# Optimization experiments

Hardware: AMD Instinct MI355X
Metric: run time of the kernel (lower is better)

## Reference

```python
import jax, jax.numpy as jnp
import numpy as np

T, D, H, HD = 2048, 2048, 16, 128
ROPE_BASE = 10000.0
NEG = jnp.float32(-1e30)


def rms_norm(x):
    # F.rms_norm(x, (x.size(-1),)) with default eps = dtype eps
    eps = jnp.finfo(x.dtype).eps
    return x * jax.lax.rsqrt(jnp.mean(x * x, axis=-1, keepdims=True) + eps)


def rotary(x):
    # x: [1, T, H, hd]; half-split rotation as in Rotary.forward
    hd = x.shape[-1]
    inv_freq = (1.0 / ROPE_BASE) ** (jnp.arange(0, hd, 2, dtype=jnp.float32) / hd)
    t = jnp.arange(x.shape[1], dtype=jnp.float32)
    freqs = jnp.outer(t, inv_freq)                      # [T, hd/2]
    cos = jnp.cos(freqs)[None, :, None, :]
    sin = jnp.sin(freqs)[None, :, None, :]
    x1, x2 = jnp.split(x, 2, axis=-1)
    return jnp.concatenate([x1 * cos + x2 * sin, -x1 * sin + x2 * cos], axis=-1)


def setup_inputs() -> dict:
    key = jax.random.key(0)
    ks = jax.random.split(key, 10)
    w = lambda k, shape: jax.random.normal(k, shape, jnp.float32) * 0.02
    return {
        "x":  jax.random.normal(ks[0], (1, T, D), jnp.float32),
        "vi": jax.random.normal(ks[1], (1, T, H, HD), jnp.float32),
        "x0": jax.random.normal(ks[2], (1, T, D), jnp.float32),
        "wq": w(ks[3], (D, D)),
        "wk": w(ks[4], (D, D)),
        "wv": w(ks[5], (D, D)),
        "wo": w(ks[6], (D, D)),
        "lamb": jnp.float32(0.5),
        "lambdas": jnp.array([1.0, 0.0], jnp.float32),
        "w_fc": w(ks[7], (4 * D, D)),
        "w_proj": w(ks[8], (D, 4 * D)),
    }


def reference(x, vi, x0, wq, wk, wv, wo, lamb, lambdas, w_fc, w_proj):
    # Block: residual blend with initial embedding x0
    xb = lambdas[0] * x + lambdas[1] * x0
    xn = rms_norm(xb)

    # --- CausalSelfAttention ---
    q = (xn @ wq.T).reshape(1, T, H, HD)
    k = (xn @ wk.T).reshape(1, T, H, HD)
    v = (xn @ wv.T).reshape(1, T, H, HD)
    v = (1.0 - lamb) * v + lamb * vi                     # value-embedding blend
    q = rotary(rms_norm(q))
    k = rotary(rms_norm(k))

    scale = 1.0 / jnp.sqrt(jnp.float32(HD))              # flex_attention default scale
    scores = jnp.einsum('bqhd,bkhd->bhqk', q, k) * scale # [1,H,T,T]
    causal = jnp.tril(jnp.ones((T, T), bool))
    scores = jnp.where(causal[None, None], scores, NEG)
    attn = jax.nn.softmax(scores, axis=-1)
    y = jnp.einsum('bhqk,bkhd->bqhd', attn, v).reshape(1, T, D)
    a = y @ wo.T                                         # attention output REPLACES x (no residual)

    # --- MLP with squared ReLU ---
    h = rms_norm(a) @ w_fc.T
    h = jnp.square(jax.nn.relu(h))
    out = a + h @ w_proj.T
    return out
```

## Files before the change

### kernel.cpp

```cpp
#include <hip/hip_runtime.h>
#include <hip/hip_bf16.h>

typedef __bf16 bf16;
typedef __bf16 bf16x8 __attribute__((ext_vector_type(8)));
typedef float f32x4 __attribute__((ext_vector_type(4)));
typedef unsigned int u32x4 __attribute__((ext_vector_type(4)));

#define DD 2048
#define DD2 4194304ull
#define G9_LDS 131072
#define G10_LDS 65536

__device__ __forceinline__ void glds16(const void* g, void* l) {
  __builtin_amdgcn_global_load_lds((const __attribute__((address_space(1))) void*)g,
                                   (__attribute__((address_space(3))) void*)l, 16, 0, 0);
}

__device__ __forceinline__ f32x4 mfma16(bf16x8 a, bf16x8 b, f32x4 c) {
  return __builtin_amdgcn_mfma_f32_16x16x32_bf16(a, b, c, 0, 0, 0);
}

__device__ __forceinline__ unsigned pk2(float lo, float hi) {
  unsigned short a = __builtin_bit_cast(unsigned short, (bf16)lo);
  unsigned short b = __builtin_bit_cast(unsigned short, (bf16)hi);
  return (unsigned)a | ((unsigned)b << 16);
}

__device__ __forceinline__ void cvt_body(const float* s0, const float* s1, const float* s2,
                                         const float* s3, bf16* dst, int seglog, size_t total,
                                         int bid, int nb) {
  size_t i = ((size_t)bid * 256 + threadIdx.x) * 16;
  const size_t stride = (size_t)nb * 256 * 16;
  for (; i < total; i += stride) {
    int seg = (int)(i >> seglog);
    const float* src = (seg == 0) ? s0 : (seg == 1) ? s1 : (seg == 2) ? s2 : s3;
    size_t loc = i - ((size_t)seg << seglog);
    float4 a0 = *(const float4*)(src + loc);
    float4 a1 = *(const float4*)(src + loc + 4);
    float4 a2 = *(const float4*)(src + loc + 8);
    float4 a3 = *(const float4*)(src + loc + 12);
    bf16x8 o0, o1;
    o0[0] = (bf16)a0.x; o0[1] = (bf16)a0.y; o0[2] = (bf16)a0.z; o0[3] = (bf16)a0.w;
    o0[4] = (bf16)a1.x; o0[5] = (bf16)a1.y; o0[6] = (bf16)a1.z; o0[7] = (bf16)a1.w;
    o1[0] = (bf16)a2.x; o1[1] = (bf16)a2.y; o1[2] = (bf16)a2.z; o1[3] = (bf16)a2.w;
    o1[4] = (bf16)a3.x; o1[5] = (bf16)a3.y; o1[6] = (bf16)a3.z; o1[7] = (bf16)a3.w;
    *(bf16x8*)(dst + i) = o0;
    *(bf16x8*)(dst + i + 8) = o1;
  }
}

__global__ __launch_bounds__(256) void pre_k(const float* __restrict__ wq, const float* __restrict__ wk,
                                             const float* __restrict__ wv, const float* __restrict__ wo,
                                             bf16* __restrict__ wdst,
                                             const float* __restrict__ x, const float* __restrict__ x0,
                                             const float* __restrict__ lambdas, bf16* __restrict__ xn) {
  if (blockIdx.x < 2048) {
    cvt_body(wq, wk, wv, wo, wdst, 22, 4 * DD2, blockIdx.x, 2048);
    return;
  }
  const int t = blockIdx.x - 2048, tid = threadIdx.x;
  const float4* xr = (const float4*)(x + (size_t)t * DD);
  float4 a0 = xr[2 * tid], a1 = xr[2 * tid + 1];
  float v[8] = {a0.x, a0.y, a0.z, a0.w, a1.x, a1.y, a1.z, a1.w};
  const float l0 = lambdas[0], l1 = lambdas[1];
  const float4* yr = (const float4*)(x0 + (size_t)t * DD);
  float4 b0 = yr[2 * tid], b1 = yr[2 * tid + 1];
  float w[8] = {b0.x, b0.y, b0.z, b0.w, b1.x, b1.y, b1.z, b1.w};
#pragma unroll
  for (int i = 0; i < 8; ++i) v[i] = l0 * v[i] + l1 * w[i];
  float ss = 0.f;
#pragma unroll
  for (int i = 0; i < 8; ++i) ss += v[i] * v[i];
#pragma unroll
  for (int off = 1; off < 64; off <<= 1) ss += __shfl_xor(ss, off, 64);
  __shared__ float red[4];
  if ((tid & 63) == 0) red[tid >> 6] = ss;
  __syncthreads();
  ss = red[0] + red[1] + red[2] + red[3];
  const float sc = rsqrtf(ss * (1.0f / DD) + 1.1920928955078125e-07f);
  bf16x8 o;
#pragma unroll
  for (int i = 0; i < 8; ++i) o[i] = (bf16)(v[i] * sc);
  *(bf16x8*)(xn + (size_t)t * DD + tid * 8) = o;
}

__global__ __launch_bounds__(256) void ropevt_k(bf16* __restrict__ qg, bf16* __restrict__ kg,
                                                const bf16* __restrict__ v, bf16* __restrict__ vt) {
  __shared__ alignas(16) bf16 tile[16 * 128];
  if (blockIdx.x < 16384) {
    const int tid = threadIdx.x, lane = tid & 63, wid = tid >> 6;
    const int p = blockIdx.x * 4 + wid;
    bf16* base = ((p >> 15) ? kg : qg);
    const int t = (p >> 4) & 2047, hh = p & 15;
    base += (size_t)t * DD + hh * 128;
    float x1 = (float)base[lane], x2 = (float)base[lane + 64];
    float ss = x1 * x1 + x2 * x2;
#pragma unroll
    for (int off = 1; off < 64; off <<= 1) ss += __shfl_xor(ss, off, 64);
    const float sc = rsqrtf(ss * (1.0f / 128.0f) + 1.1920928955078125e-07f);
    x1 *= sc; x2 *= sc;
    const float fr = (float)t * exp2f((float)lane * (-13.287712379549449f / 64.0f));
    const float s = sinf(fr), c = cosf(fr);
    base[lane]      = (bf16)(x1 * c + x2 * s);
    base[lane + 64] = (bf16)(-x1 * s + x2 * c);
    return;
  }
  const int b = blockIdx.x - 16384;
  const int tb = b & 127, hb = b >> 7, tid = threadIdx.x;
  glds16(v + (size_t)(tb * 16 + (tid >> 4)) * DD + hb * 128 + (tid & 15) * 8, tile + tid * 8);
  __syncthreads();
  const int d_l = tid & 127, tc = tid >> 7;
  bf16x8 o;
#pragma unroll
  for (int i = 0; i < 8; ++i) o[i] = tile[(tc * 8 + i) * 128 + d_l];
  *(bf16x8*)(vt + (size_t)(hb * 128 + d_l) * DD + tb * 16 + tc * 8) = o;
}

__device__ __forceinline__ void g9_stageA(const bf16* A, int Kstride, int row0, int k0,
                                          bf16* buf, int hm, int tid) {
#pragma unroll
  for (int i = 0; i < 2; ++i) {
    int e = tid + i * 512;
    int prl = e >> 3, slot = e & 7;
    int wm = prl >> 6, r63 = prl & 63;
    glds16(A + (size_t)(row0 + wm * 128 + hm * 64 + r63) * Kstride + k0 + ((slot ^ (prl & 7)) * 8),
           buf + hm * 8192 + e * 8);
  }
}
__device__ __forceinline__ void g9_stageB(const bf16* B, int Kstride, int col0, int k0,
                                          bf16* buf, int hn, int tid) {
#pragma unroll
  for (int i = 0; i < 2; ++i) {
    int e = tid + i * 512;
    int pbl = e >> 3, slot = e & 7;
    int wn = pbl >> 5, q = pbl & 31;
    glds16(B + (size_t)(col0 + wn * 64 + hn * 32 + q) * Kstride + k0 + ((slot ^ (pbl & 7)) * 8),
           buf + 16384 + hn * 8192 + e * 8);
  }
}

__device__ __forceinline__ void gemm9_core(const bf16* __restrict__ A, const bf16* __restrict__ B,
                                           int Kstride, int Klen, int row0, int col0,
                                           bf16* smem, f32x4 (&acc)[8][4]) {
  const int tid = threadIdx.x, lane = tid & 63, wid = tid >> 6;
  const int wm = wid >> 2, wn = wid & 3;
  const int l15 = lane & 15, g = lane >> 4;
  const int sw = l15 & 7;
  const int NT = Klen >> 6;
  g9_stageA(A, Kstride, row0, 0, smem, 0, tid);
  g9_stageB(B, Kstride, col0, 0, smem, 0, tid);
  g9_stageB(B, Kstride, col0, 0, smem, 1, tid);
  g9_stageA(A, Kstride, row0, 0, smem, 1, tid);
  g9_stageA(A, Kstride, row0, 64, smem + 32768, 0, tid);
  g9_stageB(B, Kstride, col0, 64, smem + 32768, 0, tid);
  asm volatile("s_waitcnt vmcnt(8)" ::: "memory");
  __builtin_amdgcn_s_barrier();

  bf16x8 a[4][2], b0[2][2], b1[2][2];
  for (int t = 0; t < NT; ++t) {
    bf16* cb = smem + (t & 1) * 32768;
    bf16* nb = smem + ((t + 1) & 1) * 32768;
    const bool s1 = (t + 1) < NT, s2 = (t + 2) < NT;
#pragma unroll
    for (int mm = 0; mm < 4; ++mm)
#pragma unroll
      for (int ks = 0; ks < 2; ++ks)
        a[mm][ks] = *(const bf16x8*)(cb + (wm * 64 + mm * 16 + l15) * 64 + (((ks * 4 + g) ^ sw) * 8));
#pragma unroll
    for (int nn = 0; nn < 2; ++nn)
#pragma unroll
      for (int ks = 0; ks < 2; ++ks)
        b0[nn][ks] = *(const bf16x8*)(cb + 16384 + (wn * 32 + nn * 16 + l15) * 64 + (((ks * 4 + g) ^ sw) * 8));
    if (s1) { g9_stageB(B, Kstride, col0, (t + 1) << 6, nb, 1, tid);
              g9_stageA(A, Kstride, row0, (t + 1) << 6, nb, 1, tid);
              asm volatile("s_waitcnt vmcnt(8)" ::: "memory"); }
    else    { asm volatile("s_waitcnt vmcnt(0)" ::: "memory"); }
    __builtin_amdgcn_s_barrier();
    __builtin_amdgcn_s_setprio(1);
#pragma unroll
    for (int mm = 0; mm < 4; ++mm)
#pragma unroll
      for (int nn = 0; nn < 2; ++nn)
#pragma unroll
        for (int ks = 0; ks < 2; ++ks)
          acc[mm][nn] = mfma16(a[mm][ks], b0[nn][ks], acc[mm][nn]);
    __builtin_amdgcn_s_setprio(0);
#pragma unroll
    for (int nn = 0; nn < 2; ++nn)
#pragma unroll
      for (int ks = 0; ks < 2; ++ks)
        b1[nn][ks] = *(const bf16x8*)(cb + 16384 + 8192 + (wn * 32 + nn * 16 + l15) * 64 + (((ks * 4 + g) ^ sw) * 8));
    __builtin_amdgcn_s_barrier();
    __builtin_amdgcn_s_setprio(1);
#pragma unroll
    for (int mm = 0; mm < 4; ++mm)
#pragma unroll
      for (int nn = 0; nn < 2; ++nn)
#pragma unroll
        for (int ks = 0; ks < 2; ++ks)
          acc[mm][2 + nn] = mfma16(a[mm][ks], b1[nn][ks], acc[mm][2 + nn]);
    __builtin_amdgcn_s_setprio(0);
#pragma unroll
    for (int mm = 0; mm < 4; ++mm)
#pragma unroll
      for (int ks = 0; ks < 2; ++ks)
        a[mm][ks] = *(const bf16x8*)(cb + 8192 + (wm * 64 + mm * 16 + l15) * 64 + (((ks * 4 + g) ^ sw) * 8));
    __builtin_amdgcn_s_barrier();
    __builtin_amdgcn_s_setprio(1);
#pragma unroll
    for (int mm = 0; mm < 4; ++mm)
#pragma unroll
      for (int nn = 0; nn < 2; ++nn)
#pragma unroll
        for (int ks = 0; ks < 2; ++ks)
          acc[4 + mm][nn] = mfma16(a[mm][ks], b0[nn][ks], acc[4 + mm][nn]);
    __builtin_amdgcn_s_setprio(0);
    if (s2) { g9_stageA(A, Kstride, row0, (t + 2) << 6, cb, 0, tid);
              g9_stageB(B, Kstride, col0, (t + 2) << 6, cb, 0, tid);
              asm volatile("s_waitcnt vmcnt(8)" ::: "memory"); }
    else if (s1) { asm volatile("s_waitcnt vmcnt(4)" ::: "memory"); }
    __builtin_amdgcn_s_barrier();
    __builtin_amdgcn_s_setprio(1);
#pragma unroll
    for (int mm = 0; mm < 4; ++mm)
#pragma unroll
      for (int nn = 0; nn < 2; ++nn)
#pragma unroll
        for (int ks = 0; ks < 2; ++ks)
          acc[4 + mm][2 + nn] = mfma16(a[mm][ks], b1[nn][ks], acc[4 + mm][2 + nn]);
    __builtin_amdgcn_s_setprio(0);
  }
}

#define GEMM9_EPI(STMT)                                                        \
  { const int lane_ = threadIdx.x & 63, wid_ = threadIdx.x >> 6;               \
    const int l15_ = lane_ & 15, g_ = lane_ >> 4;                              \
    const int wm_ = wid_ >> 2, wn_ = wid_ & 3;                                 \
    _Pragma("unroll") for (int m = 0; m < 8; ++m)                              \
    _Pragma("unroll") for (int n = 0; n < 4; ++n)                              \
    _Pragma("unroll") for (int j = 0; j < 4; ++j) {                            \
      int grow = row0 + wm_ * 128 + (m >> 2) * 64 + (m & 3) * 16 + g_ * 4 + j; \
      int gcol = col0 + wn_ * 64 + (n >> 1) * 32 + (n & 1) * 16 + l15_;        \
      float vacc = acc[m][n][j];                                               \
      STMT; } }

__global__ __launch_bounds__(512, 1) void gemm9_qkv(const bf16* __restrict__ A,
    const bf16* __restrict__ Wq, const bf16* __restrict__ Wk, const bf16* __restrict__ Wv,
    bf16* __restrict__ oq, bf16* __restrict__ ok, bf16* __restrict__ ov,
    const float* __restrict__ vi, const float* __restrict__ lambp) {
  extern __shared__ bf16 smem9[];
  const int z = blockIdx.z;
  const bf16* B = (z == 0) ? Wq : (z == 1) ? Wk : Wv;
  bf16* out = (z == 0) ? oq : (z == 1) ? ok : ov;
  const int row0 = blockIdx.y * 256, col0 = blockIdx.x * 256;
  f32x4 acc[8][4] = {};
  gemm9_core(A, B, DD, DD, row0, col0, smem9, acc);
  if (z < 2) {
    GEMM9_EPI( out[(size_t)grow * DD + gcol] = (bf16)vacc; )
  } else {
    const float lam = *lambp;
    GEMM9_EPI( out[(size_t)grow * DD + gcol] =
                 (bf16)((1.0f - lam) * vacc + lam * vi[(size_t)grow * DD + gcol]); )
  }
}

__global__ __launch_bounds__(512, 1) void gemm9_relu(const bf16* __restrict__ A, const bf16* __restrict__ B,
                                                     bf16* __restrict__ out, int N, int Kstride, int Klen) {
  extern __shared__ bf16 smem9[];
  const int row0 = blockIdx.y * 256, col0 = blockIdx.x * 256;
  f32x4 acc[8][4] = {};
  gemm9_core(A, B, Kstride, Klen, row0, col0, smem9, acc);
  GEMM9_EPI( float r = fmaxf(vacc, 0.f); out[(size_t)grow * N + gcol] = (bf16)(r * r); )
}

__global__ __launch_bounds__(512, 1) void gemm9_part(const bf16* __restrict__ A, const bf16* __restrict__ B,
                                                     float* __restrict__ o1, float* __restrict__ o2,
                                                     int zsw, int N, int Kstride, int Klen) {
  extern __shared__ bf16 smem9[];
  const int row0 = blockIdx.y * 256, col0 = blockIdx.x * 256;
  const int z = blockIdx.z, kofs = z * Klen;
  float* out = (z < zsw) ? (o1 + (size_t)z * DD2) : (o2 + (size_t)(z - zsw) * DD2);
  f32x4 acc[8][4] = {};
  gemm9_core(A + kofs, B + kofs, Kstride, Klen, row0, col0, smem9, acc);
  GEMM9_EPI( out[(size_t)grow * N + gcol] = vacc; )
}

__device__ __forceinline__ void g10_stageA(const bf16* A, int Kstride, int row0, int k0,
                                           bf16* buf, int hm, int tid) {
  int prl = tid >> 3, slot = tid & 7;
  int wmb = prl >> 5, r31 = prl & 31;
  glds16(A + (size_t)(row0 + wmb * 64 + hm * 32 + r31) * Kstride + k0 + ((slot ^ (prl & 7)) * 8),
         buf + hm * 4096 + tid * 8);
}
__device__ __forceinline__ void g10_stageB(const bf16* B, int Kstride, int col0, int k0,
                                           bf16* buf, int hn, int tid) {
  int pbl = tid >> 3, slot = tid & 7;
  int wnb = pbl >> 4, c15 = pbl & 15;
  glds16(B + (size_t)(col0 + wnb * 32 + hn * 16 + c15) * Kstride + k0 + ((slot ^ (pbl & 7)) * 8),
         buf + 8192 + hn * 4096 + tid * 8);
}

__device__ __forceinline__ void gemm10_core(const bf16* __restrict__ A, const bf16* __restrict__ B,
                                            int Kstride, int Klen, int row0, int col0,
                                            bf16* smem, f32x4 (&acc)[4][2]) {
  const int tid = threadIdx.x, lane = tid & 63, wid = tid >> 6;
  const int wm = wid >> 2, wn = wid & 3;
  const int l15 = lane & 15, g = lane >> 4;
  const int NT = Klen >> 6;
  g10_stageA(A, Kstride, row0, 0, smem, 0, tid);
  g10_stageB(B, Kstride, col0, 0, smem, 0, tid);
  g10_stageB(B, Kstride, col0, 0, smem, 1, tid);
  g10_stageA(A, Kstride, row0, 0, smem, 1, tid);
  asm volatile("s_waitcnt vmcnt(2)" ::: "memory");
  __builtin_amdgcn_s_barrier();

  bf16x8 a[2][2], b0[2], b1[2];
  for (int t = 0; t < NT; ++t) {
    bf16* cb = smem + (t & 1) * 16384;
    bf16* nb = smem + ((t + 1) & 1) * 16384;
    const int kst = (t + 1) << 6;
    const bool st = (t + 1) < NT;
#pragma unroll
    for (int mm = 0; mm < 2; ++mm)
#pragma unroll
      for (int ks = 0; ks < 2; ++ks) {
        int pr = wm * 32 + mm * 16 + l15;
        a[mm][ks] = *(const bf16x8*)(cb + pr * 64 + (((ks * 4 + g) ^ (pr & 7)) * 8));
      }
#pragma unroll
    for (int ks = 0; ks < 2; ++ks) {
      int pb = wn * 16 + l15;
      b0[ks] = *(const bf16x8*)(cb + 8192 + pb * 64 + (((ks * 4 + g) ^ (pb & 7)) * 8));
    }
    if (st) { g10_stageA(A, Kstride, row0, kst, nb, 0, tid);
              asm volatile("s_waitcnt vmcnt(2)" ::: "memory"); }
    else    { asm volatile("s_waitcnt vmcnt(1)" ::: "memory"); }
    __builtin_amdgcn_s_barrier();
    __builtin_amdgcn_s_setprio(1);
#pragma unroll
    for (int mm = 0; mm < 2; ++mm)
#pragma unroll
      for (int ks = 0; ks < 2; ++ks)
        acc[mm][0] = mfma16(a[mm][ks], b0[ks], acc[mm][0]);
    __builtin_amdgcn_s_setprio(0);
#pragma unroll
    for (int ks = 0; ks < 2; ++ks) {
      int pb = wn * 16 + l15;
      b1[ks] = *(const bf16x8*)(cb + 8192 + 4096 + pb * 64 + (((ks * 4 + g) ^ (pb & 7)) * 8));
    }
    if (st) { g10_stageB(B, Kstride, col0, kst, nb, 0, tid);
              asm volatile("s_waitcnt vmcnt(2)" ::: "memory"); }
    else    { asm volatile("s_waitcnt vmcnt(0)" ::: "memory"); }
    __builtin_amdgcn_s_barrier();
    __builtin_amdgcn_s_setprio(1);
#pragma unroll
    for (int mm = 0; mm < 2; ++mm)
#pragma unroll
      for (int ks = 0; ks < 2; ++ks)
        acc[mm][1] = mfma16(a[mm][ks], b1[ks], acc[mm][1]);
    __builtin_amdgcn_s_setprio(0);
#pragma unroll
    for (int mm = 0; mm < 2; ++mm)
#pragma unroll
      for (int ks = 0; ks < 2; ++ks) {
        int pr = 64 + wm * 32 + mm * 16 + l15;
        a[mm][ks] = *(const bf16x8*)(cb + pr * 64 + (((ks * 4 + g) ^ (pr & 7)) * 8));
      }
    if (st) g10_stageB(B, Kstride, col0, kst, nb, 1, tid);
    __builtin_amdgcn_s_barrier();
    __builtin_amdgcn_s_setprio(1);
#pragma unroll
    for (int mm = 0; mm < 2; ++mm)
#pragma unroll
      for (int ks = 0; ks < 2; ++ks)
        acc[2 + mm][0] = mfma16(a[mm][ks], b0[ks], acc[2 + mm][0]);
    __builtin_amdgcn_s_setprio(0);
    if (st) { g10_stageA(A, Kstride, row0, kst, nb, 1, tid);
              asm volatile("s_waitcnt vmcnt(2)" ::: "memory"); }
    __builtin_amdgcn_s_barrier();
    __builtin_amdgcn_s_setprio(1);
#pragma unroll
    for (int mm = 0; mm < 2; ++mm)
#pragma unroll
      for (int ks = 0; ks < 2; ++ks)
        acc[2 + mm][1] = mfma16(a[mm][ks], b1[ks], acc[2 + mm][1]);
    __builtin_amdgcn_s_setprio(0);
  }
}

#define GEMM10_EPI(STMT)                                                       \
  { const int lane_ = threadIdx.x & 63, wid_ = threadIdx.x >> 6;               \
    const int l15_ = lane_ & 15, g_ = lane_ >> 4;                              \
    const int wm_ = wid_ >> 2, wn_ = wid_ & 3;                                 \
    _Pragma("unroll") for (int m = 0; m < 4; ++m)                              \
    _Pragma("unroll") for (int n = 0; n < 2; ++n)                              \
    _Pragma("unroll") for (int j = 0; j < 4; ++j) {                            \
      int grow = row0 + wm_ * 64 + (m >> 1) * 32 + (m & 1) * 16 + g_ * 4 + j;  \
      int gcol = col0 + wn_ * 32 + n * 16 + l15_;                              \
      float vacc = acc[m][n][j];                                               \
      STMT; } }

__global__ __launch_bounds__(512, 4) void gemm10_part(const bf16* __restrict__ A, const bf16* __restrict__ B,
                                                      float* __restrict__ o1, int N, int Kstride, int Klen) {
  extern __shared__ bf16 smem10[];
  const int row0 = blockIdx.y * 128, col0 = blockIdx.x * 128;
  const int kofs = blockIdx.z * Klen;
  float* out = o1 + (size_t)blockIdx.z * DD2;
  f32x4 acc[4][2] = {};
  gemm10_core(A + kofs, B + kofs, Kstride, Klen, row0, col0, smem10, acc);
  GEMM10_EPI( out[(size_t)grow * N + gcol] = vacc; )
}

__global__ __launch_bounds__(256) void wored_cvt_k(const float* __restrict__ pa,
                                                   float* __restrict__ a_f, bf16* __restrict__ an,
                                                   const float* __restrict__ wfc, const float* __restrict__ wpj,
                                                   bf16* __restrict__ wdst) {
  if (blockIdx.x >= 2048) {
    cvt_body(wfc, wpj, wfc, wfc, wdst, 24, 8 * DD2, blockIdx.x - 2048, 2048);
    return;
  }
  const int t = blockIdx.x, tid = threadIdx.x;
  const size_t base = (size_t)t * DD + tid * 8;
  float v[8];
#pragma unroll
  for (int h = 0; h < 2; ++h) {
    size_t i = base + h * 4;
    float4 r0 = *(const float4*)(pa + i);
    float4 r1 = *(const float4*)(pa + DD2 + i);
    v[h*4+0] = r0.x + r1.x;
    v[h*4+1] = r0.y + r1.y;
    v[h*4+2] = r0.z + r1.z;
    v[h*4+3] = r0.w + r1.w;
  }
  *(float4*)(a_f + base)     = make_float4(v[0], v[1], v[2], v[3]);
  *(float4*)(a_f + base + 4) = make_float4(v[4], v[5], v[6], v[7]);
  float ss = 0.f;
#pragma unroll
  for (int i = 0; i < 8; ++i) ss += v[i] * v[i];
#pragma unroll
  for (int off = 1; off < 64; off <<= 1) ss += __shfl_xor(ss, off, 64);
  __shared__ float red[4];
  if ((tid & 63) == 0) red[tid >> 6] = ss;
  __syncthreads();
  ss = red[0] + red[1] + red[2] + red[3];
  const float sc = rsqrtf(ss * (1.0f / DD) + 1.1920928955078125e-07f);
  bf16x8 o;
#pragma unroll
  for (int i = 0; i < 8; ++i) o[i] = (bf16)(v[i] * sc);
  *(bf16x8*)(an + base) = o;
}

__global__ __launch_bounds__(256) void proj_red(const float* __restrict__ pa, const float* __restrict__ pw,
                                                const float* __restrict__ a_f, float* __restrict__ out) {
  const size_t base = ((size_t)blockIdx.x * 256 + threadIdx.x) * 8;
#pragma unroll
  for (int h = 0; h < 2; ++h) {
    size_t i = base + h * 4;
    float4 r = *(const float4*)(a_f + i);
    float4 u = *(const float4*)(pa + i);
    float4 w = *(const float4*)(pa + DD2 + i);
    float4 z = *(const float4*)(pa + 2 * DD2 + i);
    float4 y = *(const float4*)(pw + i);
    *(float4*)(out + i) = make_float4(r.x + u.x + w.x + z.x + y.x,
                                      r.y + u.y + w.y + z.y + y.y,
                                      r.z + u.z + w.z + z.z + y.z,
                                      r.w + u.w + w.w + z.w + y.w);
  }
}

__device__ __forceinline__ void att_stageK(const bf16* kg, int h, int kt, bf16* dst, int tid) {
#pragma unroll
  for (int r = 0; r < 2; ++r) {
    int e = tid + r * 256, row = e >> 4, slot = e & 15;
    glds16(kg + (size_t)(kt * 32 + row) * DD + h * 128 + ((slot ^ (row & 7)) * 8), dst + e * 8);
  }
}
__device__ __forceinline__ void att_stageV(const bf16* vtg, int h, int kt, bf16* dst, int tid) {
#pragma unroll
  for (int r = 0; r < 2; ++r) {
    int e = tid + r * 256, d = e >> 2, slot = e & 3;
    glds16(vtg + (size_t)(h * 128 + d) * DD + kt * 32 + ((slot ^ ((d >> 1) & 3)) * 8), dst + e * 8);
  }
}

__global__ __launch_bounds__(256) void attn_k(const bf16* __restrict__ qg, const bf16* __restrict__ kg,
                                              const bf16* __restrict__ vtg, bf16* __restrict__ yg) {
  __shared__ alignas(16) bf16 Ks[3][32 * 128];
  __shared__ alignas(16) bf16 Vt[3][128 * 32];
  const int h = blockIdx.y;
  const int qb = (blockIdx.y < 8) ? (31 - blockIdx.x) : blockIdx.x;
  const int tid = threadIdx.x, lane = tid & 63, wid = tid >> 6;
  const int l15 = lane & 15, g = lane >> 4, swl = l15 & 7;
  const int qrow = qb * 64 + wid * 16;
  const float scale = 0.08838834764831845f;
  bf16x8 aQ[4];
  {
    const bf16* qp = qg + (size_t)(qrow + l15) * DD + h * 128 + g * 8;
#pragma unroll
    for (int kc = 0; kc < 4; ++kc) aQ[kc] = *(const bf16x8*)(qp + kc * 32);
  }
  f32x4 acc[8] = {};
  float lsum = 0.f;
  const int nkt = qb * 2 + 2;
  att_stageK(kg, h, 0, Ks[0], tid);
  att_stageV(vtg, h, 0, Vt[0], tid);
  att_stageK(kg, h, 1, Ks[1], tid);
  att_stageV(vtg, h, 1, Vt[1], tid);
  asm volatile("s_waitcnt vmcnt(4)" ::: "memory");
  __builtin_amdgcn_s_barrier();
  int cur = 0;
  for (int kt = 0; kt < nkt; ++kt) {
    const int kbase = kt * 32;
    const int nb = (cur >= 1) ? cur - 1 : 2;
    bf16x8 kf0[4], kf1[4];
#pragma unroll
    for (int kc = 0; kc < 4; ++kc) {
      kf0[kc] = *(const bf16x8*)(Ks[cur] + l15 * 128 + (((kc * 4 + g) ^ swl) * 8));
      kf1[kc] = *(const bf16x8*)(Ks[cur] + (16 + l15) * 128 + (((kc * 4 + g) ^ swl) * 8));
    }
    if (kt + 2 < nkt) { att_stageK(kg, h, kt + 2, Ks[nb], tid);
                        att_stageV(vtg, h, kt + 2, Vt[nb], tid); }
    f32x4 S0 = {}, S1 = {};
#pragma unroll
    for (int kc = 0; kc < 4; ++kc) {
      S0 = mfma16(kf0[kc], aQ[kc], S0);
      S1 = mfma16(kf1[kc], aQ[kc], S1);
    }
    const int q = qrow + l15;
    float p0[4], p1[4];
#pragma unroll
    for (int j = 0; j < 4; ++j) {
      int k0 = kbase + 4 * g + j;
      p0[j] = (k0 <= q) ? __expf(S0[j] * scale) : 0.f;
      p1[j] = (k0 + 16 <= q) ? __expf(S1[j] * scale) : 0.f;
      lsum += p0[j] + p1[j];
    }
    unsigned w0 = pk2(p0[0], p0[1]), w1 = pk2(p0[2], p0[3]);
    unsigned w2 = pk2(p1[0], p1[1]), w3 = pk2(p1[2], p1[3]);
    const int s0l = (g & 1) * 32 + l15, s1l = s0l + 16;
    const bool hi = g >= 2;
    unsigned t00 = __shfl(w0, s0l, 64), t10 = __shfl(w1, s0l, 64);
    unsigned t01 = __shfl(w0, s1l, 64), t11 = __shfl(w1, s1l, 64);
    unsigned u00 = __shfl(w2, s0l, 64), u10 = __shfl(w3, s0l, 64);
    unsigned u01 = __shfl(w2, s1l, 64), u11 = __shfl(w3, s1l, 64);
    u32x4 av = { hi ? u00 : t00, hi ? u10 : t10, hi ? u01 : t01, hi ? u11 : t11 };
    bf16x8 aP = __builtin_bit_cast(bf16x8, av);
#pragma unroll
    for (int dt = 0; dt < 8; ++dt) {
      int d = dt * 16 + l15;
      bf16x8 bV = *(const bf16x8*)(Vt[cur] + d * 32 + ((g ^ ((d >> 1) & 3)) * 8));
      acc[dt] = mfma16(aP, bV, acc[dt]);
    }
    if (kt + 1 < nkt) {
      if (kt + 2 < nkt) { asm volatile("s_waitcnt vmcnt(4)" ::: "memory"); }
      else              { asm volatile("s_waitcnt vmcnt(0)" ::: "memory"); }
      __builtin_amdgcn_s_barrier();
    }
    cur = (cur == 2) ? 0 : cur + 1;
  }
  lsum += __shfl_xor(lsum, 16, 64);
  lsum += __shfl_xor(lsum, 32, 64);
  f32x4 linv;
#pragma unroll
  for (int j = 0; j < 4; ++j) linv[j] = 1.0f / __shfl(lsum, 4 * g + j, 64);
#pragma unroll
  for (int dt = 0; dt < 8; ++dt)
#pragma unroll
    for (int j = 0; j < 4; ++j) {
      int q = qrow + 4 * g + j;
      yg[(size_t)q * DD + h * 128 + dt * 16 + l15] = (bf16)(acc[dt][j] * linv[j]);
    }
}

extern "C" void kernel_launch(void* const* d_in, const int* in_sizes, int n_in,
                              void* d_out, int out_size, void* d_ws, size_t ws_size,
                              hipStream_t stream) {
  const float* x       = (const float*)d_in[0];
  const float* vi      = (const float*)d_in[1];
  const float* x0      = (const float*)d_in[2];
  const float* wq      = (const float*)d_in[3];
  const float* wk      = (const float*)d_in[4];
  const float* wv      = (const float*)d_in[5];
  const float* wo      = (const float*)d_in[6];
  const float* lamb    = (const float*)d_in[7];
  const float* lambdas = (const float*)d_in[8];
  const float* wfc     = (const float*)d_in[9];
  const float* wproj   = (const float*)d_in[10];
  float* out = (float*)d_out;

  (void)hipFuncSetAttribute(reinterpret_cast<const void*>(gemm9_qkv),
                            hipFuncAttributeMaxDynamicSharedMemorySize, G9_LDS);
  (void)hipFuncSetAttribute(reinterpret_cast<const void*>(gemm9_relu),
                            hipFuncAttributeMaxDynamicSharedMemorySize, G9_LDS);
  (void)hipFuncSetAttribute(reinterpret_cast<const void*>(gemm9_part),
                            hipFuncAttributeMaxDynamicSharedMemorySize, G9_LDS);
  (void)hipFuncSetAttribute(reinterpret_cast<const void*>(gemm10_part),
                            hipFuncAttributeMaxDynamicSharedMemorySize, G10_LDS);

  char* wsb = (char*)d_ws;
  size_t off = 0;
  auto alloc = [&](size_t bytes) { void* p = wsb + off; off = (off + bytes + 255) & ~(size_t)255; return p; };
  bf16* wq_b  = (bf16*)alloc(DD2 * 2);
  bf16* wk_b  = (bf16*)alloc(DD2 * 2);
  bf16* wv_b  = (bf16*)alloc(DD2 * 2);
  bf16* wo_b  = (bf16*)alloc(DD2 * 2);
  bf16* wfc_b = (bf16*)alloc(DD2 * 8);
  bf16* wpj_b = (bf16*)alloc(DD2 * 8);
  bf16* xn_b  = (bf16*)alloc(DD2 * 2);
  bf16* q_b   = (bf16*)alloc(DD2 * 2);
  bf16* k_b   = (bf16*)alloc(DD2 * 2);
  bf16* v_b   = (bf16*)alloc(DD2 * 2);
  bf16* y_b   = (bf16*)alloc(DD2 * 2);
  bf16* an_b  = (bf16*)alloc(DD2 * 2);
  float* partA = (float*)xn_b;
  float* a_f  = (float*)alloc(DD2 * 4);
  bf16* h_b   = (bf16*)alloc(DD2 * 8);
  bf16* vt_b  = h_b;

  pre_k<<<4096, 256, 0, stream>>>(wq, wk, wv, wo, (bf16*)wsb, x, x0, lambdas, xn_b);
  gemm9_qkv<<<dim3(8, 8, 3), 512, G9_LDS, stream>>>(xn_b, wq_b, wk_b, wv_b, q_b, k_b, v_b, vi, lamb);
  ropevt_k<<<18432, 256, 0, stream>>>(q_b, k_b, v_b, vt_b);
  attn_k<<<dim3(32, 16), 256, 0, stream>>>(q_b, k_b, vt_b, y_b);
  gemm10_part<<<dim3(16, 16, 2), 512, G10_LDS, stream>>>(y_b, wo_b, partA, DD, DD, 1024);
  wored_cvt_k<<<4096, 256, 0, stream>>>(partA, a_f, an_b, wfc, wproj, wfc_b);
  gemm9_relu<<<dim3(32, 8), 512, G9_LDS, stream>>>(an_b, wfc_b, h_b, 4 * DD, DD, DD);
  gemm9_part<<<dim3(8, 8, 4), 512, G9_LDS, stream>>>(h_b, wpj_b, partA, (float*)wfc_b, 3, DD, 4 * DD, 2048);
  proj_red<<<2048, 256, 0, stream>>>(partA, (float*)wfc_b, a_f, out);
}
```

Measured before the change: 360.5 us.

## Widen attention KV tiles to 64 keys with double buffering

The attention kernel now processes 64 keys per iteration instead of 32, using two LDS buffers of 64-row K and V^T tiles rather than three 32-row buffers. This halves the number of loop iterations, barriers and waitcnts per query block, and gives each iteration more MFMA work to hide latency. The cost is shallower prefetch (one tile ahead instead of two), a full vmcnt(0) wait each step, and a larger LDS footprint per block that may reduce occupancy. The V swizzle is changed to match the 64-wide rows.

```diff
diff --git a/kernel.cpp b/kernel.cpp
--- a/kernel.cpp
+++ b/kernel.cpp
@@ -468,25 +468,25 @@
   }
 }
 
-__device__ __forceinline__ void att_stageK(const bf16* kg, int h, int kt, bf16* dst, int tid) {
-#pragma unroll
-  for (int r = 0; r < 2; ++r) {
+__device__ __forceinline__ void att_stageK64(const bf16* kg, int h, int kt, bf16* dst, int tid) {
+#pragma unroll
+  for (int r = 0; r < 4; ++r) {
     int e = tid + r * 256, row = e >> 4, slot = e & 15;
-    glds16(kg + (size_t)(kt * 32 + row) * DD + h * 128 + ((slot ^ (row & 7)) * 8), dst + e * 8);
-  }
-}
-__device__ __forceinline__ void att_stageV(const bf16* vtg, int h, int kt, bf16* dst, int tid) {
-#pragma unroll
-  for (int r = 0; r < 2; ++r) {
-    int e = tid + r * 256, d = e >> 2, slot = e & 3;
-    glds16(vtg + (size_t)(h * 128 + d) * DD + kt * 32 + ((slot ^ ((d >> 1) & 3)) * 8), dst + e * 8);
+    glds16(kg + (size_t)(kt * 64 + row) * DD + h * 128 + ((slot ^ (row & 7)) * 8), dst + e * 8);
+  }
+}
+__device__ __forceinline__ void att_stageV64(const bf16* vtg, int h, int kt, bf16* dst, int tid) {
+#pragma unroll
+  for (int r = 0; r < 4; ++r) {
+    int e = tid + r * 256, d = e >> 3, slot = e & 7;
+    glds16(vtg + (size_t)(h * 128 + d) * DD + kt * 64 + ((slot ^ (d & 7)) * 8), dst + e * 8);
   }
 }
 
 __global__ __launch_bounds__(256) void attn_k(const bf16* __restrict__ qg, const bf16* __restrict__ kg,
                                               const bf16* __restrict__ vtg, bf16* __restrict__ yg) {
-  __shared__ alignas(16) bf16 Ks[3][32 * 128];
-  __shared__ alignas(16) bf16 Vt[3][128 * 32];
+  __shared__ alignas(16) bf16 Ks[2][64 * 128];
+  __shared__ alignas(16) bf16 Vt[2][128 * 64];
   const int h = blockIdx.y;
   const int qb = (blockIdx.y < 8) ? (31 - blockIdx.x) : blockIdx.x;
   const int tid = threadIdx.x, lane = tid & 63, wid = tid >> 6;
@@ -501,62 +501,64 @@
   }
   f32x4 acc[8] = {};
   float lsum = 0.f;
-  const int nkt = qb * 2 + 2;
-  att_stageK(kg, h, 0, Ks[0], tid);
-  att_stageV(vtg, h, 0, Vt[0], tid);
-  att_stageK(kg, h, 1, Ks[1], tid);
-  att_stageV(vtg, h, 1, Vt[1], tid);
-  asm volatile("s_waitcnt vmcnt(4)" ::: "memory");
+  const int nkt = qb + 1;
+  att_stageK64(kg, h, 0, Ks[0], tid);
+  att_stageV64(vtg, h, 0, Vt[0], tid);
+  asm volatile("s_waitcnt vmcnt(0)" ::: "memory");
   __builtin_amdgcn_s_barrier();
-  int cur = 0;
   for (int kt = 0; kt < nkt; ++kt) {
-    const int kbase = kt * 32;
-    const int nb = (cur >= 1) ? cur - 1 : 2;
-    bf16x8 kf0[4], kf1[4];
+    const int cur = kt & 1, nb = cur ^ 1;
+    if (kt + 1 < nkt) { att_stageK64(kg, h, kt + 1, Ks[nb], tid);
+                        att_stageV64(vtg, h, kt + 1, Vt[nb], tid); }
+    f32x4 S[4] = {};
 #pragma unroll
     for (int kc = 0; kc < 4; ++kc) {
-      kf0[kc] = *(const bf16x8*)(Ks[cur] + l15 * 128 + (((kc * 4 + g) ^ swl) * 8));
-      kf1[kc] = *(const bf16x8*)(Ks[cur] + (16 + l15) * 128 + (((kc * 4 + g) ^ swl) * 8));
-    }
-    if (kt + 2 < nkt) { att_stageK(kg, h, kt + 2, Ks[nb], tid);
-                        att_stageV(vtg, h, kt + 2, Vt[nb], tid); }
-    f32x4 S0 = {}, S1 = {};
-#pragma unroll
-    for (int kc = 0; kc < 4; ++kc) {
-      S0 = mfma16(kf0[kc], aQ[kc], S0);
-      S1 = mfma16(kf1[kc], aQ[kc], S1);
+#pragma unroll
+      for (int s = 0; s < 4; ++s) {
+        bf16x8 kf = *(const bf16x8*)(Ks[cur] + (16 * s + l15) * 128 + (((kc * 4 + g) ^ swl) * 8));
+        S[s] = mfma16(kf, aQ[kc], S[s]);
+      }
     }
     const int q = qrow + l15;
-    float p0[4], p1[4];
-#pragma unroll
-    for (int j = 0; j < 4; ++j) {
-      int k0 = kbase + 4 * g + j;
-      p0[j] = (k0 <= q) ? __expf(S0[j] * scale) : 0.f;
-      p1[j] = (k0 + 16 <= q) ? __expf(S1[j] * scale) : 0.f;
-      lsum += p0[j] + p1[j];
+    float p[4][4];
+    unsigned pw[4][2];
+#pragma unroll
+    for (int s = 0; s < 4; ++s) {
+#pragma unroll
+      for (int j = 0; j < 4; ++j) {
+        int k0 = kt * 64 + 16 * s + 4 * g + j;
+        p[s][j] = (k0 <= q) ? __expf(S[s][j] * scale) : 0.f;
+        lsum += p[s][j];
+      }
+      pw[s][0] = pk2(p[s][0], p[s][1]);
+      pw[s][1] = pk2(p[s][2], p[s][3]);
     }
-    unsigned w0 = pk2(p0[0], p0[1]), w1 = pk2(p0[2], p0[3]);
-    unsigned w2 = pk2(p1[0], p1[1]), w3 = pk2(p1[2], p1[3]);
-    const int s0l = (g & 1) * 32 + l15, s1l = s0l + 16;
-    const bool hi = g >= 2;
-    unsigned t00 = __shfl(w0, s0l, 64), t10 = __shfl(w1, s0l, 64);
-    unsigned t01 = __shfl(w0, s1l, 64), t11 = __shfl(w1, s1l, 64);
-    unsigned u00 = __shfl(w2, s0l, 64), u10 = __shfl(w3, s0l, 64);
-    unsigned u01 = __shfl(w2, s1l, 64), u11 = __shfl(w3, s1l, 64);
-    u32x4 av = { hi ? u00 : t00, hi ? u10 : t10, hi ? u01 : t01, hi ? u11 : t11 };
-    bf16x8 aP = __builtin_bit_cast(bf16x8, av);
+    const int lane_lo = (2 * (g & 1)) * 16 + l15, lane_hi = lane_lo + 16;
+    const bool ghi = g >= 2;
+    unsigned a0l = __shfl(pw[0][0], lane_lo), a1l = __shfl(pw[1][0], lane_lo);
+    unsigned b0l = __shfl(pw[0][1], lane_lo), b1l = __shfl(pw[1][1], lane_lo);
+    unsigned a0h = __shfl(pw[0][0], lane_hi), a1h = __shfl(pw[1][0], lane_hi);
+    unsigned b0h = __shfl(pw[0][1], lane_hi), b1h = __shfl(pw[1][1], lane_hi);
+    u32x4 av0 = { ghi ? a1l : a0l, ghi ? b1l : b0l, ghi ? a1h : a0h, ghi ? b1h : b0h };
+    unsigned c0l = __shfl(pw[2][0], lane_lo), c1l = __shfl(pw[3][0], lane_lo);
+    unsigned d0l = __shfl(pw[2][1], lane_lo), d1l = __shfl(pw[3][1], lane_lo);
+    unsigned c0h = __shfl(pw[2][0], lane_hi), c1h = __shfl(pw[3][0], lane_hi);
+    unsigned d0h = __shfl(pw[2][1], lane_hi), d1h = __shfl(pw[3][1], lane_hi);
+    u32x4 av1 = { ghi ? c1l : c0l, ghi ? d1l : d0l, ghi ? c1h : c0h, ghi ? d1h : d0h };
+    bf16x8 aP0 = __builtin_bit_cast(bf16x8, av0);
+    bf16x8 aP1 = __builtin_bit_cast(bf16x8, av1);
 #pragma unroll
     for (int dt = 0; dt < 8; ++dt) {
       int d = dt * 16 + l15;
-      bf16x8 bV = *(const bf16x8*)(Vt[cur] + d * 32 + ((g ^ ((d >> 1) & 3)) * 8));
-      acc[dt] = mfma16(aP, bV, acc[dt]);
+      bf16x8 bV0 = *(const bf16x8*)(Vt[cur] + d * 64 + ((g ^ (d & 7)) * 8));
+      bf16x8 bV1 = *(const bf16x8*)(Vt[cur] + d * 64 + (((4 + g) ^ (d & 7)) * 8));
+      acc[dt] = mfma16(aP0, bV0, acc[dt]);
+      acc[dt] = mfma16(aP1, bV1, acc[dt]);
     }
     if (kt + 1 < nkt) {
-      if (kt + 2 < nkt) { asm volatile("s_waitcnt vmcnt(4)" ::: "memory"); }
-      else              { asm volatile("s_waitcnt vmcnt(0)" ::: "memory"); }
+      asm volatile("s_waitcnt vmcnt(0)" ::: "memory");
       __builtin_amdgcn_s_barrier();
     }
-    cur = (cur == 2) ? 0 : cur + 1;
   }
   lsum += __shfl_xor(lsum, 16, 64);
   lsum += __shfl_xor(lsum, 32, 64);
```

Result: no change. 361.8 us (+0.4%).
